# Kernel tuning notes

Hardware: AMD Instinct MI355X
Metric: run time of the kernel (lower is better)

## Reference

```python
import jax, jax.numpy as jnp
import numpy as np

NEG_INF = jnp.finfo(jnp.float32).min


def setup_inputs() -> dict:
    key = jax.random.key(0)
    k1, k2, k3, k4 = jax.random.split(key, 4)
    B, T, C, H = 8, 2048, 1024, 128
    x = jax.random.normal(k1, (B, T, C), dtype=jnp.float32)
    # nn.Linear(n_embd, head_size, bias=False) -> weight [head_size, n_embd]
    s = 1.0 / np.sqrt(C)
    Wk = jax.random.normal(k2, (H, C), dtype=jnp.float32) * s
    Wq = jax.random.normal(k3, (H, C), dtype=jnp.float32) * s
    Wv = jax.random.normal(k4, (H, C), dtype=jnp.float32) * s
    return {"x": x, "Wk": Wk, "Wq": Wq, "Wv": Wv}


def reference(x, Wk, Wq, Wv):
    B, T, C = x.shape
    # projections: x [B,T,C] @ W.T [C,H] -> [B,T,H]
    k = jnp.einsum('btc,hc->bth', x, Wk)
    q = jnp.einsum('btc,hc->bth', x, Wq)
    v = jnp.einsum('btc,hc->bth', x, Wv)
    # NOTE: original scales by C**-0.5 (input channels), faithful here
    scores = jnp.einsum('bqh,bkh->bqk', q, k) * (C ** -0.5)
    causal = jnp.tril(jnp.ones((T, T), dtype=bool))  # tril[:T,:T]
    scores = jnp.where(causal, scores, NEG_INF)
    attn = jax.nn.softmax(scores, axis=-1)
    # dropout(p=0.1) is identity in eval mode; omitted for deterministic reference
    out = jnp.einsum('bqk,bkh->bqh', attn, v)
    return out
```

## Files before the change

kernel.cpp:

```cpp
#include <hip/hip_runtime.h>
#include <hip/hip_bf16.h>

#define B_ 8
#define T_ 2048
#define C_ 1024
#define H_ 128
#define M_ (B_ * T_)

typedef __bf16 bf16x8 __attribute__((ext_vector_type(8)));
typedef __bf16 bf16x4v __attribute__((ext_vector_type(4)));
typedef float f32x4 __attribute__((ext_vector_type(4)));

static __device__ __forceinline__ bf16x8 cvt8(float4 a, float4 b) {
    bf16x8 r;
    r[0] = (__bf16)a.x; r[1] = (__bf16)a.y; r[2] = (__bf16)a.z; r[3] = (__bf16)a.w;
    r[4] = (__bf16)b.x; r[5] = (__bf16)b.y; r[6] = (__bf16)b.z; r[7] = (__bf16)b.w;
    return r;
}


__global__ __launch_bounds__(256) void wprep_kernel(
    const float* __restrict__ Wq, const float* __restrict__ Wk,
    const float* __restrict__ Wv, __bf16* __restrict__ wb)
{
    const int i = blockIdx.x * 256 + threadIdx.x;
    const int w = i >> 15;
    const int jj = i & 32767;
    const float* s = (w == 0) ? Wq : (w == 1) ? Wk : Wv;
    float4 v = ((const float4*)s)[jj];
    bf16x4v o;
    o[0] = (__bf16)v.x; o[1] = (__bf16)v.y; o[2] = (__bf16)v.z; o[3] = (__bf16)v.w;
    *(bf16x4v*)(wb + ((size_t)w << 17) + (size_t)jj * 4) = o;
}

__global__ __launch_bounds__(256) void proj_fused(
    const float* __restrict__ x, const __bf16* __restrict__ wb,
    __bf16* __restrict__ qb, __bf16* __restrict__ kb, __bf16* __restrict__ vTb)
{
    __shared__ __align__(16) __bf16 As[64 * 64];
    __shared__ __align__(16) __bf16 Bs[128 * 64];

    const int tid = threadIdx.x;
    const int lane = tid & 63;
    const int wid = tid >> 6;
    const int bx = blockIdx.x;
    const int base24 = bx / 24;
    const int rem24 = bx % 24;
    const int which = rem24 >> 3;
    const int mt = base24 * 8 + (rem24 & 7);
    const int m0 = mt * 64;
    const int n0 = which * 128;

    const int wr = wid >> 1;
    const int wc = wid & 1;
    const int fr = lane & 15;
    const int g4 = lane >> 4;
    const int rbase = g4 * 4;
    const int sw8 = fr & 7;

    f32x4 acc[2][4];
#pragma unroll
    for (int i = 0; i < 2; i++)
#pragma unroll
        for (int j = 0; j < 4; j++) acc[i][j] = (f32x4){0.f, 0.f, 0.f, 0.f};

    for (int kt = 0; kt < 16; kt++) {
        const int k0 = kt * 64;

#pragma unroll
        for (int c = 0; c < 2; c++) {
            const int chunk = c * 256 + tid;
            const int arow = chunk >> 3;
            const int aslot = chunk & 7;
            const float* xs = x + (size_t)(m0 + arow) * C_ + k0 + aslot * 8;
            float4 xa = *(const float4*)xs;
            float4 xb2 = *(const float4*)(xs + 4);
            *(bf16x8*)&As[arow * 64 + ((aslot ^ (arow & 7)) << 3)] = cvt8(xa, xb2);
        }
#pragma unroll
        for (int i = 0; i < 4; i++) {
            const int chunk = i * 256 + tid;
            const int brow = chunk >> 3;
            const int bsrc = ((chunk & 7) ^ (brow & 7)) << 3;
            __builtin_amdgcn_global_load_lds(
                (const __attribute__((address_space(1))) void*)(wb + (size_t)(n0 + brow) * C_ + k0 + bsrc),
                (__attribute__((address_space(3))) void*)&Bs[chunk * 8], 16, 0, 0);
        }
        __syncthreads();

#pragma unroll
        for (int kk = 0; kk < 2; kk++) {
            const int sc = kk * 4 + g4;
            const int soff = (sc ^ sw8) << 3;
            bf16x8 ar[2], br[4];
#pragma unroll
            for (int i = 0; i < 2; i++)
                ar[i] = *(const bf16x8*)&As[(wr * 32 + i * 16 + fr) * 64 + soff];
#pragma unroll
            for (int j = 0; j < 4; j++)
                br[j] = *(const bf16x8*)&Bs[(wc * 64 + j * 16 + fr) * 64 + soff];
#pragma unroll
            for (int i = 0; i < 2; i++)
#pragma unroll
                for (int j = 0; j < 4; j++)
                    acc[i][j] = __builtin_amdgcn_mfma_f32_16x16x32_bf16(ar[i], br[j], acc[i][j], 0, 0, 0);
        }
        __syncthreads();
    }

#pragma unroll
    for (int i = 0; i < 2; i++) {
#pragma unroll
        for (int j = 0; j < 4; j++) {
            const int h = wc * 64 + j * 16 + fr;
#pragma unroll
            for (int rr = 0; rr < 4; rr++) {
                const int row = m0 + wr * 32 + i * 16 + rbase + rr;
                const __bf16 val = (__bf16)acc[i][j][rr];
                if (which == 0) {
                    qb[(size_t)row * H_ + h] = val;
                } else if (which == 1) {
                    kb[(size_t)row * H_ + h] = val;
                } else {
                    const int bb = row >> 11;
                    const int tt = row & (T_ - 1);
                    vTb[((size_t)bb * H_ + h) * T_ + tt] = val;
                }
            }
        }
    }
}

__global__ __launch_bounds__(512) void attn_fused(
    const __bf16* __restrict__ qb, const __bf16* __restrict__ kb,
    const __bf16* __restrict__ vTb,
    unsigned int* __restrict__ acc_ws, float* __restrict__ m_ws,
    float* __restrict__ l_ws)
{
    __shared__ __align__(16) __bf16 Klds[2][32 * 128];
    __shared__ __align__(16) __bf16 Vlds[2][128 * 32];
    __shared__ __align__(16) __bf16 pbuf[8][2][16][32];

    const int tid = threadIdx.x;
    const int lane = tid & 63;
    const int wid = tid >> 6;
    const int gw = blockIdx.x;
    const int b = gw & 7;
    const int j = 35 - (gw >> 3);
    int qc = 0;
#pragma unroll
    for (int q = 1; q < 8; q++) qc += (j >= (q * (q + 1)) / 2) ? 1 : 0;
    const int s = j - (qc * (qc + 1)) / 2;
    const int lo = 8 * s, hi = 8 * s + 8;

    const int qrow_loc = qc * 256 + wid * 32;
    const size_t qrow0 = (size_t)b * T_ + qrow_loc;

    const int fr = lane & 15;
    const int g4 = lane >> 4;
    const int koff = g4 * 8;
    const int rbase = g4 * 4;
    const int sw = fr & 6;

    const int krow = tid >> 4, kslot = tid & 15;
    const int vrow = tid >> 2, vslot = tid & 3;
    const __bf16* kgs = kb + ((size_t)b * T_ + krow) * H_ + ((kslot ^ (krow & 15)) << 3);
    const __bf16* vgs = vTb + ((size_t)b * H_ + vrow) * T_ + ((vslot ^ (vrow & 3)) << 3);

    bf16x8 qf[2][4];
#pragma unroll
    for (int g = 0; g < 2; g++) {
        const __bf16* Qb = qb + (qrow0 + g * 16 + fr) * H_ + koff;
#pragma unroll
        for (int hc = 0; hc < 4; hc++)
            qf[g][hc] = *(const bf16x8*)(Qb + hc * 32);
    }

    float m[2] = {-1e30f, -1e30f};
    float l[2] = {0.f, 0.f};
    f32x4 acc[2][8];
#pragma unroll
    for (int g = 0; g < 2; g++)
#pragma unroll
        for (int i = 0; i < 8; i++) acc[g][i] = (f32x4){0.f, 0.f, 0.f, 0.f};

    const float scale = 0.03125f;

    {
        const int k0 = lo * 32, nb = lo & 1;
        __builtin_amdgcn_global_load_lds(
            (const __attribute__((address_space(1))) void*)(kgs + (size_t)k0 * H_),
            (__attribute__((address_space(3))) void*)&Klds[nb][tid * 8], 16, 0, 0);
        __builtin_amdgcn_global_load_lds(
            (const __attribute__((address_space(1))) void*)(vgs + k0),
            (__attribute__((address_space(3))) void*)&Vlds[nb][tid * 8], 16, 0, 0);
    }

    for (int kt = lo; kt < hi; kt++) {
        const int k0 = kt * 32;
        const int pb = kt & 1;

        if (kt + 1 < hi) {
            const int k1 = (kt + 1) * 32, nb = (kt + 1) & 1;
            __builtin_amdgcn_global_load_lds(
                (const __attribute__((address_space(1))) void*)(kgs + (size_t)k1 * H_),
                (__attribute__((address_space(3))) void*)&Klds[nb][tid * 8], 16, 0, 0);
            __builtin_amdgcn_global_load_lds(
                (const __attribute__((address_space(1))) void*)(vgs + k1),
                (__attribute__((address_space(3))) void*)&Vlds[nb][tid * 8], 16, 0, 0);
        }
        __syncthreads();

        if (k0 <= qrow_loc + 31) {
            f32x4 sg[2][2];
#pragma unroll
            for (int g = 0; g < 2; g++) {
                sg[g][0] = (f32x4){0.f, 0.f, 0.f, 0.f};
                sg[g][1] = (f32x4){0.f, 0.f, 0.f, 0.f};
            }
            __builtin_amdgcn_s_setprio(1);
#pragma unroll
            for (int hc = 0; hc < 4; hc++) {
                const int r0 = fr, r1 = 16 + fr;
                bf16x8 kf0 = *(const bf16x8*)&Klds[pb][r0 * 128 + (((hc * 4 + g4) ^ (r0 & 15)) << 3)];
                bf16x8 kf1 = *(const bf16x8*)&Klds[pb][r1 * 128 + (((hc * 4 + g4) ^ (r1 & 15)) << 3)];
#pragma unroll
                for (int g = 0; g < 2; g++) {
                    sg[g][0] = __builtin_amdgcn_mfma_f32_16x16x32_bf16(kf0, qf[g][hc], sg[g][0], 0, 0, 0);
                    sg[g][1] = __builtin_amdgcn_mfma_f32_16x16x32_bf16(kf1, qf[g][hc], sg[g][1], 0, 0, 0);
                }
            }
            __builtin_amdgcn_s_setprio(0);

            float tv[2];
#pragma unroll
            for (int g = 0; g < 2; g++) {
                const int qrow = qrow_loc + g * 16 + fr;
                float t = -1e30f;
#pragma unroll
                for (int h = 0; h < 2; h++) {
#pragma unroll
                    for (int r = 0; r < 4; r++) {
                        const int key = k0 + h * 16 + rbase + r;
                        float v = sg[g][h][r] * scale;
                        v = (key > qrow) ? -1e30f : v;
                        sg[g][h][r] = v;
                        t = fmaxf(t, v);
                    }
                }
                t = fmaxf(t, __shfl_xor(t, 16));
                t = fmaxf(t, __shfl_xor(t, 32));
                tv[g] = t;
            }

            const bool need = (tv[0] > m[0] + 8.0f) || (tv[1] > m[1] + 8.0f);
            if (__any(need)) {
#pragma unroll
                for (int g = 0; g < 2; g++) {
                    const float mnew = fmaxf(m[g], tv[g]);
                    const float corr = __expf(m[g] - mnew);
                    l[g] *= corr;
#pragma unroll
                    for (int r = 0; r < 4; r++) {
                        const float cr = __shfl(corr, rbase + r);
#pragma unroll
                        for (int ht = 0; ht < 8; ht++) acc[g][ht][r] *= cr;
                    }
                    m[g] = mnew;
                }
            }

#pragma unroll
            for (int g = 0; g < 2; g++) {
                bf16x4v p0, p1;
                float sum = 0.f;
#pragma unroll
                for (int r = 0; r < 4; r++) {
                    const float e0 = __expf(sg[g][0][r] - m[g]);
                    const float e1 = __expf(sg[g][1][r] - m[g]);
                    p0[r] = (__bf16)e0;
                    p1[r] = (__bf16)e1;
                    sum += e0 + e1;
                }
                sum += __shfl_xor(sum, 16);
                sum += __shfl_xor(sum, 32);
                l[g] += sum;
                *(bf16x4v*)&pbuf[wid][g][fr][((g4) ^ sw) * 4] = p0;
                *(bf16x4v*)&pbuf[wid][g][fr][((4 + g4) ^ sw) * 4] = p1;
            }

            bf16x8 pa[2];
#pragma unroll
            for (int g = 0; g < 2; g++)
                pa[g] = *(const bf16x8*)&pbuf[wid][g][fr][((2 * g4) ^ sw) * 4];

            __builtin_amdgcn_s_setprio(1);
#pragma unroll
            for (int ht = 0; ht < 8; ht++) {
                const int vr = ht * 16 + fr;
                bf16x8 vf = *(const bf16x8*)&Vlds[pb][vr * 32 + ((g4 ^ (vr & 3)) << 3)];
#pragma unroll
                for (int g = 0; g < 2; g++)
                    acc[g][ht] = __builtin_amdgcn_mfma_f32_16x16x32_bf16(pa[g], vf, acc[g][ht], 0, 0, 0);
            }
            __builtin_amdgcn_s_setprio(0);
        }
        __syncthreads();
    }

#pragma unroll
    for (int g = 0; g < 2; g++) {
        const size_t row0 = qrow0 + g * 16;
#pragma unroll
        for (int p = 0; p < 4; p++) {
#pragma unroll
            for (int r = 0; r < 4; r++) {
                const __bf16 lo2 = (__bf16)acc[g][2 * p][r];
                const __bf16 hi2 = (__bf16)acc[g][2 * p + 1][r];
                const unsigned int w =
                    ((unsigned int)*(const unsigned short*)&hi2 << 16) |
                    *(const unsigned short*)&lo2;
                acc_ws[((size_t)s * M_ + row0 + rbase + r) * 64 + p * 16 + fr] = w;
            }
        }
    }

    if (lane < 16) {
#pragma unroll
        for (int g = 0; g < 2; g++) {
            const size_t row = qrow0 + g * 16 + lane;
            m_ws[(size_t)s * M_ + row] = m[g];
            l_ws[(size_t)s * M_ + row] = l[g];
        }
    }
}

__global__ __launch_bounds__(256) void attn_merge_bal(
    const unsigned int* __restrict__ acc_ws, const float* __restrict__ m_ws,
    const float* __restrict__ l_ws, float* __restrict__ out)
{
    const int lane = threadIdx.x & 63;
    const int g = blockIdx.x * 4 + (threadIdx.x >> 6);
    const int c = 1 + ((g >> 8) & 7);

    float mm = -1e30f;
    for (int s = 0; s < c; s++)
        mm = fmaxf(mm, m_ws[(size_t)s * M_ + g]);
    float ll = 0.f;
    for (int s = 0; s < c; s++)
        ll += l_ws[(size_t)s * M_ + g] * __expf(m_ws[(size_t)s * M_ + g] - mm);
    const float inv = 1.0f / ll;

    float ox = 0.f, oy = 0.f;
    for (int s = 0; s < c; s++) {
        const float sc = __expf(m_ws[(size_t)s * M_ + g] - mm);
        const unsigned int w = acc_ws[((size_t)s * M_ + g) * 64 + lane];
        ox += __uint_as_float((w & 0xffffu) << 16) * sc;
        oy += __uint_as_float(w & 0xffff0000u) * sc;
    }
    ox *= inv; oy *= inv;
    const int col0 = ((lane >> 4) << 5) + (lane & 15);
    out[(size_t)g * H_ + col0] = ox;
    out[(size_t)g * H_ + col0 + 16] = oy;
}

__global__ __launch_bounds__(64) void proj_kernel(
    const float* __restrict__ x,
    const float* __restrict__ Wq, const float* __restrict__ Wk,
    const float* __restrict__ Wv,
    __bf16* __restrict__ qb, __bf16* __restrict__ kb, __bf16* __restrict__ vTb)
{
    const int lane = threadIdx.x;
    const int gw = blockIdx.x;
    const int which = gw >> 10;
    const int mt = gw & 1023;
    const float* W = (which == 0) ? Wq : (which == 1) ? Wk : Wv;
    const int fr = lane & 15;
    const int koff = (lane >> 4) * 8;
    const float* xrow = x + (size_t)(mt * 16 + fr) * C_ + koff;
    const float* wbase = W + (size_t)fr * C_ + koff;
    f32x4 acc[8];
#pragma unroll
    for (int i = 0; i < 8; i++) acc[i] = (f32x4){0.f, 0.f, 0.f, 0.f};
    for (int kc = 0; kc < C_; kc += 32) {
        float4 xa = *(const float4*)(xrow + kc);
        float4 xb2 = *(const float4*)(xrow + kc + 4);
        bf16x8 af = cvt8(xa, xb2);
#pragma unroll
        for (int ht = 0; ht < 8; ht++) {
            const float* wrow = wbase + (size_t)ht * 16 * C_ + kc;
            float4 wa = *(const float4*)(wrow);
            float4 wb2 = *(const float4*)(wrow + 4);
            bf16x8 bfr = cvt8(wa, wb2);
            acc[ht] = __builtin_amdgcn_mfma_f32_16x16x32_bf16(af, bfr, acc[ht], 0, 0, 0);
        }
    }
    const int rbase = (lane >> 4) * 4;
#pragma unroll
    for (int ht = 0; ht < 8; ht++) {
#pragma unroll
        for (int r = 0; r < 4; r++) {
            int row = mt * 16 + rbase + r;
            int h = ht * 16 + fr;
            __bf16 val = (__bf16)acc[ht][r];
            if (which == 0) qb[(size_t)row * H_ + h] = val;
            else if (which == 1) kb[(size_t)row * H_ + h] = val;
            else {
                int bb = row >> 11; int tt = row & (T_ - 1);
                vTb[((size_t)bb * H_ + h) * T_ + tt] = val;
            }
        }
    }
}

__global__ __launch_bounds__(64) void attn_kernel(
    const __bf16* __restrict__ qb, const __bf16* __restrict__ kb,
    const __bf16* __restrict__ vTb, float* __restrict__ out)
{
    __shared__ __align__(16) __bf16 plds[16][32];
    const int lane = threadIdx.x;
    const int gw = blockIdx.x;
    const int b = gw >> 7;
    const int qt = gw & 127;
    const int q0 = qt * 16;
    const int fr = lane & 15;
    const int koff = (lane >> 4) * 8;
    const int rbase = (lane >> 4) * 4;
    const __bf16* Qbase = qb + ((size_t)b * T_ + q0 + fr) * H_ + koff;
    bf16x8 qf[4];
#pragma unroll
    for (int hc = 0; hc < 4; hc++) qf[hc] = *(const bf16x8*)(Qbase + hc * 32);
    float m[4], l[4];
    f32x4 acc[8];
#pragma unroll
    for (int r = 0; r < 4; r++) { m[r] = -1e30f; l[r] = 0.f; }
#pragma unroll
    for (int i = 0; i < 8; i++) acc[i] = (f32x4){0.f, 0.f, 0.f, 0.f};
    const int nkt = (q0 + 15) / 32 + 1;
    const float scale = 0.03125f;
    for (int kt = 0; kt < nkt; kt++) {
        const int k0 = kt * 32;
        f32x4 s0 = (f32x4){0.f, 0.f, 0.f, 0.f};
        f32x4 s1 = (f32x4){0.f, 0.f, 0.f, 0.f};
        const __bf16* Kb0 = kb + ((size_t)b * T_ + k0 + fr) * H_ + koff;
        const __bf16* Kb1 = Kb0 + 16 * H_;
#pragma unroll
        for (int hc = 0; hc < 4; hc++) {
            bf16x8 kf0 = *(const bf16x8*)(Kb0 + hc * 32);
            s0 = __builtin_amdgcn_mfma_f32_16x16x32_bf16(qf[hc], kf0, s0, 0, 0, 0);
            bf16x8 kf1 = *(const bf16x8*)(Kb1 + hc * 32);
            s1 = __builtin_amdgcn_mfma_f32_16x16x32_bf16(qf[hc], kf1, s1, 0, 0, 0);
        }
#pragma unroll
        for (int r = 0; r < 4; r++) {
            const int qrow = q0 + rbase + r;
            float v0 = s0[r] * scale;
            float v1 = s1[r] * scale;
            if (k0 + fr > qrow)      v0 = -1e30f;
            if (k0 + 16 + fr > qrow) v1 = -1e30f;
            float mx = fmaxf(v0, v1);
#pragma unroll
            for (int d = 1; d < 16; d <<= 1) mx = fmaxf(mx, __shfl_xor(mx, d));
            const float mnew = fmaxf(m[r], mx);
            const float corr = __expf(m[r] - mnew);
            const float e0 = __expf(v0 - mnew);
            const float e1 = __expf(v1 - mnew);
            float rs = e0 + e1;
#pragma unroll
            for (int d = 1; d < 16; d <<= 1) rs += __shfl_xor(rs, d);
            l[r] = l[r] * corr + rs;
            m[r] = mnew;
#pragma unroll
            for (int ht = 0; ht < 8; ht++) acc[ht][r] *= corr;
            plds[rbase + r][fr] = (__bf16)e0;
            plds[rbase + r][16 + fr] = (__bf16)e1;
        }
        __syncthreads();
        bf16x8 pa = *(const bf16x8*)(&plds[fr][koff]);
        const __bf16* Vb = vTb + ((size_t)b * H_ + fr) * T_ + k0 + koff;
#pragma unroll
        for (int ht = 0; ht < 8; ht++) {
            bf16x8 vf = *(const bf16x8*)(Vb + (size_t)ht * 16 * T_);
            acc[ht] = __builtin_amdgcn_mfma_f32_16x16x32_bf16(pa, vf, acc[ht], 0, 0, 0);
        }
        __syncthreads();
    }
    float inv[4];
#pragma unroll
    for (int r = 0; r < 4; r++) inv[r] = 1.0f / l[r];
    float* obase = out + ((size_t)b * T_ + q0 + rbase) * H_ + fr;
#pragma unroll
    for (int ht = 0; ht < 8; ht++) {
#pragma unroll
        for (int r = 0; r < 4; r++) {
            obase[(size_t)r * H_ + ht * 16] = acc[ht][r] * inv[r];
        }
    }
}

extern "C" void kernel_launch(void* const* d_in, const int* in_sizes, int n_in,
                              void* d_out, int out_size, void* d_ws, size_t ws_size,
                              hipStream_t stream) {
    const float* x  = (const float*)d_in[0];
    const float* Wk = (const float*)d_in[1];
    const float* Wq = (const float*)d_in[2];
    const float* Wv = (const float*)d_in[3];
    float* out = (float*)d_out;
    uint8_t* ws = (uint8_t*)d_ws;

    const size_t NEED = 47972352;

    if (ws_size >= NEED) {
        unsigned int* acc_ws = (unsigned int*)ws;
        __bf16* wb  = (__bf16*)(ws + 33554432);
        __bf16* qb  = (__bf16*)(ws + 34340864);
        __bf16* kb  = (__bf16*)(ws + 38535168);
        __bf16* vTb = (__bf16*)(ws + 42729472);
        float*  m_ws = (float*)(ws + 46923776);
        float*  l_ws = (float*)(ws + 47448064);

        wprep_kernel<<<384, 256, 0, stream>>>(Wq, Wk, Wv, wb);
        proj_fused<<<768, 256, 0, stream>>>(x, wb, qb, kb, vTb);
        attn_fused<<<B_ * 36, 512, 0, stream>>>(qb, kb, vTb, acc_ws, m_ws, l_ws);
        attn_merge_bal<<<M_ / 4, 256, 0, stream>>>(acc_ws, m_ws, l_ws, out);
    } else {
        __bf16* qb  = (__bf16*)d_ws;
        __bf16* kb  = qb + (size_t)M_ * H_;
        __bf16* vTb = kb + (size_t)M_ * H_;
        proj_kernel<<<3072, 64, 0, stream>>>(x, Wq, Wk, Wv, qb, kb, vTb);
        attn_kernel<<<1024, 64, 0, stream>>>(qb, kb, vTb, out);
    }
}
```

Baseline: 85.35 us.

## Load x fragments straight to registers and widen projection K-tile to 128

The projection kernel no longer stages x through shared memory. Each wave loads its own 16 rows of x from global memory directly into MFMA A-fragment registers and converts them to bf16 in registers. The K tile grows from 64 to 128, with a 16-way XOR swizzle on the weight tile, which halves the number of barrier-separated iterations. Each wave now owns 16 rows by all 128 columns instead of a 32x64 sub-tile, which trades LDS traffic and syncs for more weight-fragment LDS reads per wave and less coalesced x loads.

New measurement: 96.39 us. 12.9% more time.

```diff
diff --git a/kernel.cpp b/kernel.cpp
--- a/kernel.cpp
+++ b/kernel.cpp
@@ -37,12 +37,11 @@
     const float* __restrict__ x, const __bf16* __restrict__ wb,
     __bf16* __restrict__ qb, __bf16* __restrict__ kb, __bf16* __restrict__ vTb)
 {
-    __shared__ __align__(16) __bf16 As[64 * 64];
-    __shared__ __align__(16) __bf16 Bs[128 * 64];
+    __shared__ __align__(16) __bf16 Bs[128 * 128];
 
     const int tid = threadIdx.x;
     const int lane = tid & 63;
-    const int wid = tid >> 6;
+    const int w = tid >> 6;
     const int bx = blockIdx.x;
     const int base24 = bx / 24;
     const int rem24 = bx % 24;
@@ -51,37 +50,33 @@
     const int m0 = mt * 64;
     const int n0 = which * 128;
 
-    const int wr = wid >> 1;
-    const int wc = wid & 1;
     const int fr = lane & 15;
     const int g4 = lane >> 4;
     const int rbase = g4 * 4;
-    const int sw8 = fr & 7;
-
-    f32x4 acc[2][4];
-#pragma unroll
-    for (int i = 0; i < 2; i++)
-#pragma unroll
-        for (int j = 0; j < 4; j++) acc[i][j] = (f32x4){0.f, 0.f, 0.f, 0.f};
-
-    for (int kt = 0; kt < 16; kt++) {
-        const int k0 = kt * 64;
-
-#pragma unroll
-        for (int c = 0; c < 2; c++) {
-            const int chunk = c * 256 + tid;
-            const int arow = chunk >> 3;
-            const int aslot = chunk & 7;
-            const float* xs = x + (size_t)(m0 + arow) * C_ + k0 + aslot * 8;
-            float4 xa = *(const float4*)xs;
-            float4 xb2 = *(const float4*)(xs + 4);
-            *(bf16x8*)&As[arow * 64 + ((aslot ^ (arow & 7)) << 3)] = cvt8(xa, xb2);
-        }
-#pragma unroll
-        for (int i = 0; i < 4; i++) {
+
+    const float* xrow = x + (size_t)(m0 + w * 16 + fr) * C_ + g4 * 8;
+
+    f32x4 acc[8];
+#pragma unroll
+    for (int j = 0; j < 8; j++) acc[j] = (f32x4){0.f, 0.f, 0.f, 0.f};
+
+    for (int kt = 0; kt < 8; kt++) {
+        const int k0 = kt * 128;
+
+        float4 xa[4], xb2[4];
+#pragma unroll
+        for (int kc = 0; kc < 4; kc++) {
+            const float* xs = xrow + k0 + kc * 32;
+            xa[kc] = *(const float4*)xs;
+            xb2[kc] = *(const float4*)(xs + 4);
+        }
+
+#pragma unroll
+        for (int i = 0; i < 8; i++) {
             const int chunk = i * 256 + tid;
-            const int brow = chunk >> 3;
-            const int bsrc = ((chunk & 7) ^ (brow & 7)) << 3;
+            const int brow = chunk >> 4;
+            const int bslot = chunk & 15;
+            const int bsrc = ((bslot ^ (brow & 15)) << 3);
             __builtin_amdgcn_global_load_lds(
                 (const __attribute__((address_space(1))) void*)(wb + (size_t)(n0 + brow) * C_ + k0 + bsrc),
                 (__attribute__((address_space(3))) void*)&Bs[chunk * 8], 16, 0, 0);
@@ -89,43 +84,33 @@
         __syncthreads();
 
 #pragma unroll
-        for (int kk = 0; kk < 2; kk++) {
-            const int sc = kk * 4 + g4;
-            const int soff = (sc ^ sw8) << 3;
-            bf16x8 ar[2], br[4];
-#pragma unroll
-            for (int i = 0; i < 2; i++)
-                ar[i] = *(const bf16x8*)&As[(wr * 32 + i * 16 + fr) * 64 + soff];
-#pragma unroll
-            for (int j = 0; j < 4; j++)
-                br[j] = *(const bf16x8*)&Bs[(wc * 64 + j * 16 + fr) * 64 + soff];
-#pragma unroll
-            for (int i = 0; i < 2; i++)
-#pragma unroll
-                for (int j = 0; j < 4; j++)
-                    acc[i][j] = __builtin_amdgcn_mfma_f32_16x16x32_bf16(ar[i], br[j], acc[i][j], 0, 0, 0);
+        for (int kc = 0; kc < 4; kc++) {
+            const bf16x8 af = cvt8(xa[kc], xb2[kc]);
+#pragma unroll
+            for (int j = 0; j < 8; j++) {
+                const int rj = j * 16 + fr;
+                bf16x8 br = *(const bf16x8*)&Bs[rj * 128 + (((kc * 4 + g4) ^ fr) << 3)];
+                acc[j] = __builtin_amdgcn_mfma_f32_16x16x32_bf16(af, br, acc[j], 0, 0, 0);
+            }
         }
         __syncthreads();
     }
 
 #pragma unroll
-    for (int i = 0; i < 2; i++) {
-#pragma unroll
-        for (int j = 0; j < 4; j++) {
-            const int h = wc * 64 + j * 16 + fr;
-#pragma unroll
-            for (int rr = 0; rr < 4; rr++) {
-                const int row = m0 + wr * 32 + i * 16 + rbase + rr;
-                const __bf16 val = (__bf16)acc[i][j][rr];
-                if (which == 0) {
-                    qb[(size_t)row * H_ + h] = val;
-                } else if (which == 1) {
-                    kb[(size_t)row * H_ + h] = val;
-                } else {
-                    const int bb = row >> 11;
-                    const int tt = row & (T_ - 1);
-                    vTb[((size_t)bb * H_ + h) * T_ + tt] = val;
-                }
+    for (int j = 0; j < 8; j++) {
+        const int h = j * 16 + fr;
+#pragma unroll
+        for (int rr = 0; rr < 4; rr++) {
+            const int row = m0 + w * 16 + rbase + rr;
+            const __bf16 val = (__bf16)acc[j][rr];
+            if (which == 0) {
+                qb[(size_t)row * H_ + h] = val;
+            } else if (which == 1) {
+                kb[(size_t)row * H_ + h] = val;
+            } else {
+                const int bb = row >> 11;
+                const int tt = row & (T_ - 1);
+                vTb[((size_t)bb * H_ + h) * T_ + tt] = val;
             }
         }
     }
```
